# Kernel optimization log

Hardware: AMD Instinct MI355X
Metric: run time of the kernel (lower is better)

The kernel has to match this reference:

```python
import jax, jax.numpy as jnp
import numpy as np

D_MODEL = 1024
N_HEADS = 16
HEAD_DIM = D_MODEL // N_HEADS
EPS = 1e-5


def _rope_tables(T, dim, dtype):
    inv_freq = 1.0 / (10000.0 ** (np.arange(0, dim, 2, dtype=np.float32) / dim))
    t = np.arange(T, dtype=np.float32)
    freqs = np.einsum('i,j->ij', t, inv_freq)            # [T, dim/2]
    emb = np.concatenate([freqs, freqs], axis=-1)        # [T, dim]
    return jnp.asarray(np.cos(emb), dtype), jnp.asarray(np.sin(emb), dtype)


def _rotate(x, cos, sin):
    # x: [B, T, H, hd]; cos/sin: [T, hd] broadcast over B, H
    c = cos[None, :, None, :]
    s = sin[None, :, None, :]
    x1, x2 = jnp.split(x, 2, axis=-1)
    return x * c + jnp.concatenate([-x2, x1], axis=-1) * s


def setup_inputs() -> dict:
    key = jax.random.key(0)
    k1, k2, k3 = jax.random.split(key, 3)
    B, T = 2, 2048
    x = jax.random.normal(k1, (B, T, D_MODEL), jnp.float32)
    norm_w = jnp.ones((D_MODEL,), jnp.float32)
    w_qkv = jax.random.normal(k2, (D_MODEL, 3 * D_MODEL), jnp.float32) * (D_MODEL ** -0.5)
    w_out = jax.random.normal(k3, (D_MODEL, D_MODEL), jnp.float32) * (D_MODEL ** -0.5)
    return {"x": x, "norm_w": norm_w, "w_qkv": w_qkv, "w_out": w_out}


def reference(x, norm_w, w_qkv, w_out):
    B, T, D = x.shape
    residual = x
    # RMSNorm
    h = x * jax.lax.rsqrt(jnp.mean(x * x, axis=-1, keepdims=True) + EPS) * norm_w
    # QKV projection
    qkv = (h @ w_qkv).reshape(B, T, 3, N_HEADS, HEAD_DIM)
    q, k, v = qkv[:, :, 0], qkv[:, :, 1], qkv[:, :, 2]   # [B, T, H, hd]
    # RoPE
    cos, sin = _rope_tables(T, HEAD_DIM, x.dtype)
    q = _rotate(q, cos, sin)
    k = _rotate(k, cos, sin)
    # Non-causal scaled dot-product attention
    scale = HEAD_DIM ** -0.5
    scores = jnp.einsum('bqhd,bkhd->bhqk', q, k) * scale
    attn = jax.nn.softmax(scores, axis=-1)
    out = jnp.einsum('bhqk,bkhd->bqhd', attn, v).reshape(B, T, D)
    return residual + out @ w_out
```

## Files before the change

### kernel.cpp

```cpp
#include <hip/hip_runtime.h>
#include <hip/hip_bf16.h>

typedef float f32x4 __attribute__((ext_vector_type(4)));
typedef __bf16 bf16x8 __attribute__((ext_vector_type(8)));
typedef __bf16 bf16x4 __attribute__((ext_vector_type(4)));

#define D_MODEL 1024
#define T_SEQ   2048
#define NH      16
#define HD      64

__device__ __forceinline__ void gload16(const void* g, void* l) {
    __builtin_amdgcn_global_load_lds(
        (const __attribute__((address_space(1))) unsigned int*)g,
        (__attribute__((address_space(3))) unsigned int*)l, 16, 0, 0);
}

__global__ __launch_bounds__(256) void k_rope_table(float2* __restrict__ tab) {
    int idx = blockIdx.x * 256 + threadIdx.x;
    int t = idx >> 5, i = idx & 31;
    float inv = powf(10000.f, -(float)i * (1.f / 32.f));
    float ang = (float)t * inv;
    tab[idx] = make_float2(cosf(ang), sinf(ang));
}

__global__ __launch_bounds__(256) void k_rmsnorm(const float* __restrict__ x,
                                                 const float* __restrict__ w,
                                                 __bf16* __restrict__ h) {
    int row = blockIdx.x;
    int tid = threadIdx.x;
    const float4 v = ((const float4*)(x + (size_t)row * D_MODEL))[tid];
    float ss = v.x * v.x + v.y * v.y + v.z * v.z + v.w * v.w;
#pragma unroll
    for (int off = 32; off > 0; off >>= 1) ss += __shfl_down(ss, off, 64);
    __shared__ float red[4];
    if ((tid & 63) == 0) red[tid >> 6] = ss;
    __syncthreads();
    float total = red[0] + red[1] + red[2] + red[3];
    float rms = rsqrtf(total * (1.f / 1024.f) + 1e-5f);
    const float4 wv = ((const float4*)w)[tid];
    bf16x4 o;
    o[0] = (__bf16)(v.x * rms * wv.x);
    o[1] = (__bf16)(v.y * rms * wv.y);
    o[2] = (__bf16)(v.z * rms * wv.z);
    o[3] = (__bf16)(v.w * rms * wv.w);
    ((bf16x4*)(h + (size_t)row * D_MODEL))[tid] = o;
}

__global__ __launch_bounds__(256) void k_transpose_cast(const float* __restrict__ src,
                                                        __bf16* __restrict__ dst,
                                                        int R, int C) {
    __shared__ float tile[32][33];
    int tx = threadIdx.x & 31, ty = threadIdx.x >> 5;
    int c0 = blockIdx.x * 32, r0 = blockIdx.y * 32;
#pragma unroll
    for (int dy = 0; dy < 32; dy += 8)
        tile[ty + dy][tx] = src[(size_t)(r0 + ty + dy) * C + c0 + tx];
    __syncthreads();
#pragma unroll
    for (int dy = 0; dy < 32; dy += 8)
        dst[(size_t)(c0 + ty + dy) * R + r0 + tx] = (__bf16)tile[tx][ty + dy];
}

template <int EPI>
__global__ __launch_bounds__(256) void k_gemm(const __bf16* __restrict__ A,
                                              const __bf16* __restrict__ Bt, int K,
                                              const float2* __restrict__ tab,
                                              __bf16* __restrict__ Qr,
                                              __bf16* __restrict__ Kr,
                                              __bf16* __restrict__ Vt,
                                              const float* __restrict__ resid,
                                              float* __restrict__ outf) {
    __shared__ __bf16 ldsA[128 * 64];
    __shared__ __bf16 ldsB[128 * 64];
    const int tid  = threadIdx.x;
    const int lane = tid & 63;
    const int wave = tid >> 6;
    const int tile_m = blockIdx.y * 128;
    const int tile_n = blockIdx.x * 128;
    const int wm = (wave >> 1) * 64;
    const int wn = (wave & 1) * 64;
    f32x4 acc[4][4] = {};

    const int srow8 = lane >> 3;
    const int sslot = lane & 7;

    for (int k0 = 0; k0 < K; k0 += 64) {
#pragma unroll
        for (int i = 0; i < 4; i++) {
            int rbase = i * 32 + wave * 8;
            int row = rbase + srow8;
            int scol = (sslot ^ (row & 7)) * 8;
            gload16(A  + (size_t)(tile_m + row) * K + k0 + scol,
                    (char*)ldsA + rbase * 128);
            gload16(Bt + (size_t)(tile_n + row) * K + k0 + scol,
                    (char*)ldsB + rbase * 128);
        }
        __syncthreads();
#pragma unroll
        for (int kc = 0; kc < 2; kc++) {
            bf16x8 af[4], bfr[4];
            int s = kc * 4 + (lane >> 4);
#pragma unroll
            for (int mi = 0; mi < 4; mi++) {
                int row = wm + mi * 16 + (lane & 15);
                af[mi] = *(const bf16x8*)((char*)ldsA + row * 128 + ((s ^ (row & 7)) << 4));
            }
#pragma unroll
            for (int nf = 0; nf < 4; nf++) {
                int row = wn + nf * 16 + (lane & 15);
                bfr[nf] = *(const bf16x8*)((char*)ldsB + row * 128 + ((s ^ (row & 7)) << 4));
            }
#pragma unroll
            for (int mi = 0; mi < 4; mi++)
#pragma unroll
                for (int nf = 0; nf < 4; nf++)
                    acc[mi][nf] = __builtin_amdgcn_mfma_f32_16x16x32_bf16(
                        af[mi], bfr[nf], acc[mi][nf], 0, 0, 0);
        }
        __syncthreads();
    }

    if (EPI == 0) {
        const int nb  = tile_n + wn;
        const int sec = nb >> 10;
        const int hh  = (nb & 1023) >> 6;
        if (sec < 2) {
            __bf16* dstbase = (sec == 0) ? Qr : Kr;
            const float sc = (sec == 0) ? 0.180336880111f : 1.0f;
#pragma unroll
            for (int mi = 0; mi < 4; mi++) {
#pragma unroll
                for (int r = 0; r < 4; r++) {
                    int m = tile_m + wm + mi * 16 + (lane >> 4) * 4 + r;
                    int bb = m >> 11, t = m & 2047;
                    float2 cs0 = tab[t * 32 + (lane & 15)];
                    float2 cs1 = tab[t * 32 + 16 + (lane & 15)];
                    float x0 = acc[mi][0][r], x1 = acc[mi][1][r];
                    float x2 = acc[mi][2][r], x3 = acc[mi][3][r];
                    __bf16* dst = dstbase + ((size_t)(bb * NH + hh) * T_SEQ + t) * HD + (lane & 15);
                    dst[0]  = (__bf16)((x0 * cs0.x - x2 * cs0.y) * sc);
                    dst[16] = (__bf16)((x1 * cs1.x - x3 * cs1.y) * sc);
                    dst[32] = (__bf16)((x2 * cs0.x + x0 * cs0.y) * sc);
                    dst[48] = (__bf16)((x3 * cs1.x + x1 * cs1.y) * sc);
                }
            }
        } else {
#pragma unroll
            for (int mi = 0; mi < 4; mi++) {
                int m0 = tile_m + wm + mi * 16 + (lane >> 4) * 4;
                int bb = m0 >> 11, t0 = m0 & 2047;
#pragma unroll
                for (int nf = 0; nf < 4; nf++) {
                    int d = nf * 16 + (lane & 15);
                    bf16x4 pv;
                    pv[0] = (__bf16)acc[mi][nf][0];
                    pv[1] = (__bf16)acc[mi][nf][1];
                    pv[2] = (__bf16)acc[mi][nf][2];
                    pv[3] = (__bf16)acc[mi][nf][3];
                    *(bf16x4*)(Vt + ((size_t)(bb * NH + hh) * HD + d) * T_SEQ + t0) = pv;
                }
            }
        }
    } else {
#pragma unroll
        for (int mi = 0; mi < 4; mi++)
#pragma unroll
            for (int r = 0; r < 4; r++) {
                int m = tile_m + wm + mi * 16 + (lane >> 4) * 4 + r;
#pragma unroll
                for (int nf = 0; nf < 4; nf++) {
                    int n = tile_n + wn + nf * 16 + (lane & 15);
                    size_t idx = (size_t)m * D_MODEL + n;
                    outf[idx] = resid[idx] + acc[mi][nf][r];
                }
            }
    }
}

__global__ __launch_bounds__(256, 4) void k_attn(const __bf16* __restrict__ Qr,
                                                 const __bf16* __restrict__ Kr,
                                                 const __bf16* __restrict__ Vt,
                                                 __bf16* __restrict__ aout) {
    __shared__ __bf16 ldsK[2][64 * 64];
    __shared__ __bf16 ldsV[2][64 * 64];
    __shared__ __bf16 plds_all[4][16 * 64];
    const int lane = threadIdx.x & 63;
    const int wave = threadIdx.x >> 6;
    const int g  = lane >> 4;
    const int lr = lane & 15;

    const int lin = blockIdx.x;
    const int xcd = lin & 7;
    const int idx = lin >> 3;
    const int bh  = xcd * 4 + (idx >> 5);
    const int qb  = idx & 31;
    const int q0  = qb * 64 + wave * 16;

    const __bf16* Q  = Qr + (size_t)bh * T_SEQ * HD;
    const __bf16* Kp = Kr + (size_t)bh * T_SEQ * HD;
    const __bf16* Vp = Vt + (size_t)bh * HD * T_SEQ;
    char* plds = (char*)plds_all[wave];

    bf16x8 qf[2];
#pragma unroll
    for (int kc = 0; kc < 2; kc++)
        qf[kc] = *(const bf16x8*)(Q + (size_t)(q0 + lr) * HD + kc * 32 + g * 8);

    const int srow8 = lane >> 3;
    const int sslot = lane & 7;
    auto stage = [&](int buf, int kk) {
#pragma unroll
        for (int j = 0; j < 2; j++) {
            int c = wave * 2 + j;
            int row = c * 8 + srow8;
            int scol = (sslot ^ (row & 7)) * 8;
            gload16(Kp + (size_t)(kk + row) * HD + scol,
                    (char*)&ldsK[buf][0] + c * 1024);
            gload16(Vp + (size_t)row * T_SEQ + kk + scol,
                    (char*)&ldsV[buf][0] + c * 1024);
        }
    };

    f32x4 o[4] = {};
    float mrun = -1e30f;
    float lrun = 0.f;

    stage(0, 0);
    __syncthreads();
    int buf = 0;

    for (int tile = 0; tile < 32; tile++) {
        if (tile < 31) stage(buf ^ 1, (tile + 1) * 64);

        const char* Kb = (const char*)&ldsK[buf][0];
        const char* Vb = (const char*)&ldsV[buf][0];

        f32x4 s[4] = {};
#pragma unroll
        for (int kc = 0; kc < 2; kc++) {
            bf16x8 kf[4];
#pragma unroll
            for (int ki = 0; ki < 4; ki++) {
                int row = ki * 16 + lr;
                kf[ki] = *(const bf16x8*)(Kb + row * 128 +
                                          ((kc * 64 + g * 16) ^ ((row & 7) << 4)));
            }
#pragma unroll
            for (int ki = 0; ki < 4; ki++)
                s[ki] = __builtin_amdgcn_mfma_f32_16x16x32_bf16(
                    kf[ki], qf[kc], s[ki], 0, 0, 0);
        }

        float t0 = fmaxf(fmaxf(s[0][0], s[0][1]), fmaxf(s[0][2], s[0][3]));
        float t1 = fmaxf(fmaxf(s[1][0], s[1][1]), fmaxf(s[1][2], s[1][3]));
        float t2 = fmaxf(fmaxf(s[2][0], s[2][1]), fmaxf(s[2][2], s[2][3]));
        float t3 = fmaxf(fmaxf(s[3][0], s[3][1]), fmaxf(s[3][2], s[3][3]));
        float tv = fmaxf(fmaxf(t0, t1), fmaxf(t2, t3));
        tv = fmaxf(tv, __shfl_xor(tv, 16, 64));
        tv = fmaxf(tv, __shfl_xor(tv, 32, 64));
        float mnew = fmaxf(mrun, tv);
        float fac = __builtin_amdgcn_exp2f(mrun - mnew);
        mrun = mnew;
        float ts = 0.f;
#pragma unroll
        for (int ki = 0; ki < 4; ki++) {
            float p0 = __builtin_amdgcn_exp2f(s[ki][0] - mnew);
            float p1 = __builtin_amdgcn_exp2f(s[ki][1] - mnew);
            float p2 = __builtin_amdgcn_exp2f(s[ki][2] - mnew);
            float p3 = __builtin_amdgcn_exp2f(s[ki][3] - mnew);
            ts += (p0 + p1) + (p2 + p3);
            bf16x4 pk;
            pk[0] = (__bf16)p0; pk[1] = (__bf16)p1;
            pk[2] = (__bf16)p2; pk[3] = (__bf16)p3;
            *(bf16x4*)(plds + lr * 128 + ((ki * 32 + g * 8) ^ ((lr & 7) << 4))) = pk;
        }
        ts += __shfl_xor(ts, 16, 64);
        ts += __shfl_xor(ts, 32, 64);
        lrun = lrun * fac + ts;
        float facT[4];
#pragma unroll
        for (int r = 0; r < 4; r++)
            facT[r] = __shfl(fac, g * 4 + r, 64);
#pragma unroll
        for (int nf = 0; nf < 4; nf++)
#pragma unroll
            for (int r = 0; r < 4; r++)
                o[nf][r] *= facT[r];

#pragma unroll
        for (int kc = 0; kc < 2; kc++) {
            bf16x8 pf = *(const bf16x8*)(plds + lr * 128 +
                                         ((kc * 64 + g * 16) ^ ((lr & 7) << 4)));
            bf16x8 vf[4];
#pragma unroll
            for (int nf = 0; nf < 4; nf++) {
                int row = nf * 16 + lr;
                vf[nf] = *(const bf16x8*)(Vb + row * 128 +
                                          ((kc * 64 + g * 16) ^ ((row & 7) << 4)));
            }
#pragma unroll
            for (int nf = 0; nf < 4; nf++)
                o[nf] = __builtin_amdgcn_mfma_f32_16x16x32_bf16(
                    pf, vf[nf], o[nf], 0, 0, 0);
        }
        __syncthreads();
        buf ^= 1;
    }

    const int bb = bh >> 4, hh = bh & 15;
    float invT[4];
#pragma unroll
    for (int r = 0; r < 4; r++)
        invT[r] = 1.f / __shfl(lrun, g * 4 + r, 64);
#pragma unroll
    for (int r = 0; r < 4; r++) {
        int t = q0 + g * 4 + r;
#pragma unroll
        for (int nf = 0; nf < 4; nf++) {
            int d = nf * 16 + lr;
            aout[((size_t)(bb * T_SEQ + t)) * D_MODEL + hh * HD + d] =
                (__bf16)(o[nf][r] * invT[r]);
        }
    }
}

extern "C" void kernel_launch(void* const* d_in, const int* in_sizes, int n_in,
                              void* d_out, int out_size, void* d_ws, size_t ws_size,
                              hipStream_t stream) {
    const float* x      = (const float*)d_in[0];
    const float* norm_w = (const float*)d_in[1];
    const float* w_qkv  = (const float*)d_in[2];
    const float* w_out  = (const float*)d_in[3];
    float* out = (float*)d_out;
    char* ws = (char*)d_ws;

    __bf16* hbuf  = (__bf16*)(ws);
    __bf16* wqkvT = (__bf16*)(ws + ((size_t)8  << 20));
    __bf16* woutT = (__bf16*)(ws + ((size_t)14 << 20));
    float2* tab   = (float2*)(ws + ((size_t)16 << 20));
    __bf16* Qr    = (__bf16*)(ws + ((size_t)17 << 20));
    __bf16* Kr    = (__bf16*)(ws + ((size_t)25 << 20));
    __bf16* Vt    = (__bf16*)(ws + ((size_t)33 << 20));

    k_rope_table<<<dim3(256), dim3(256), 0, stream>>>(tab);
    k_rmsnorm<<<dim3(4096), dim3(256), 0, stream>>>(x, norm_w, hbuf);
    k_transpose_cast<<<dim3(96, 32), dim3(256), 0, stream>>>(w_qkv, wqkvT, 1024, 3072);
    k_transpose_cast<<<dim3(32, 32), dim3(256), 0, stream>>>(w_out, woutT, 1024, 1024);
    k_gemm<0><<<dim3(24, 32), dim3(256), 0, stream>>>(hbuf, wqkvT, 1024, tab,
                                                      Qr, Kr, Vt, nullptr, nullptr);
    k_attn<<<dim3(1024), dim3(256), 0, stream>>>(Qr, Kr, Vt, hbuf);
    k_gemm<1><<<dim3(8, 32), dim3(256), 0, stream>>>(hbuf, woutT, 1024, nullptr,
                                                     nullptr, nullptr, nullptr, x, out);
}
```

Baseline: 222.4 us.

## Restructure attention inner loop with lazy rescale, precomputed offsets and priorities

Reworks the flash-attention tile loop. LDS swizzle offsets and global staging pointers are computed once instead of per tile, and V fragment loads are issued early so they overlap the softmax. The online-softmax rescale is skipped unless the running max grows by more than a threshold, and s_setprio is raised around the MFMA sections. The RoPE table's powf is replaced with exp2. The lazy rescale lets exponentials go up to 2^8 before renormalising, which adds some risk of precision loss in the bf16 P values.

```diff
diff --git a/kernel.cpp b/kernel.cpp
--- a/kernel.cpp
+++ b/kernel.cpp
@@ -19,7 +19,7 @@
 __global__ __launch_bounds__(256) void k_rope_table(float2* __restrict__ tab) {
     int idx = blockIdx.x * 256 + threadIdx.x;
     int t = idx >> 5, i = idx & 31;
-    float inv = powf(10000.f, -(float)i * (1.f / 32.f));
+    float inv = __builtin_amdgcn_exp2f(-(float)i * 0.41524101186f);
     float ang = (float)t * inv;
     tab[idx] = make_float2(cosf(ang), sinf(ang));
 }
@@ -201,56 +201,77 @@
     const __bf16* Kp = Kr + (size_t)bh * T_SEQ * HD;
     const __bf16* Vp = Vt + (size_t)bh * HD * T_SEQ;
     char* plds = (char*)plds_all[wave];
+    char* Kbase = (char*)&ldsK[0][0];
+    char* Vbase = (char*)&ldsV[0][0];
+
+    int kofs[2][4], vofs[2][4], pwr[4], prd[2];
+#pragma unroll
+    for (int kc = 0; kc < 2; kc++)
+#pragma unroll
+        for (int i = 0; i < 4; i++) {
+            int row = i * 16 + lr;
+            int sw = (kc * 64 + g * 16) ^ ((row & 7) << 4);
+            kofs[kc][i] = row * 128 + sw;
+            vofs[kc][i] = row * 128 + sw;
+        }
+#pragma unroll
+    for (int ki = 0; ki < 4; ki++)
+        pwr[ki] = lr * 128 + ((ki * 32 + g * 8) ^ ((lr & 7) << 4));
+#pragma unroll
+    for (int kc = 0; kc < 2; kc++)
+        prd[kc] = lr * 128 + ((kc * 64 + g * 16) ^ ((lr & 7) << 4));
+
+    const int srow8 = lane >> 3;
+    const int sslot = lane & 7;
+    const int scol = (sslot ^ srow8) * 8;
+    const int c0 = wave * 2, c1 = wave * 2 + 1;
+    const int r0 = c0 * 8 + srow8, r1 = c1 * 8 + srow8;
+    const __bf16* kg0 = Kp + (size_t)r0 * HD + scol;
+    const __bf16* kg1 = Kp + (size_t)r1 * HD + scol;
+    const __bf16* vg0 = Vp + (size_t)r0 * T_SEQ + scol;
+    const __bf16* vg1 = Vp + (size_t)r1 * T_SEQ + scol;
+    char* Kl0 = Kbase + c0 * 1024;
+    char* Kl1 = Kbase + c1 * 1024;
+    char* Vl0 = Vbase + c0 * 1024;
+    char* Vl1 = Vbase + c1 * 1024;
 
     bf16x8 qf[2];
 #pragma unroll
     for (int kc = 0; kc < 2; kc++)
         qf[kc] = *(const bf16x8*)(Q + (size_t)(q0 + lr) * HD + kc * 32 + g * 8);
-
-    const int srow8 = lane >> 3;
-    const int sslot = lane & 7;
-    auto stage = [&](int buf, int kk) {
-#pragma unroll
-        for (int j = 0; j < 2; j++) {
-            int c = wave * 2 + j;
-            int row = c * 8 + srow8;
-            int scol = (sslot ^ (row & 7)) * 8;
-            gload16(Kp + (size_t)(kk + row) * HD + scol,
-                    (char*)&ldsK[buf][0] + c * 1024);
-            gload16(Vp + (size_t)row * T_SEQ + kk + scol,
-                    (char*)&ldsV[buf][0] + c * 1024);
-        }
-    };
 
     f32x4 o[4] = {};
     float mrun = -1e30f;
     float lrun = 0.f;
 
-    stage(0, 0);
+    gload16(kg0, Kl0); gload16(kg1, Kl1);
+    gload16(vg0, Vl0); gload16(vg1, Vl1);
+    kg0 += 64 * HD; kg1 += 64 * HD; vg0 += 64; vg1 += 64;
     __syncthreads();
-    int buf = 0;
 
     for (int tile = 0; tile < 32; tile++) {
-        if (tile < 31) stage(buf ^ 1, (tile + 1) * 64);
-
-        const char* Kb = (const char*)&ldsK[buf][0];
-        const char* Vb = (const char*)&ldsV[buf][0];
+        const int bufoff = (tile & 1) << 13;
+        if (tile < 31) {
+            const int nb = bufoff ^ 8192;
+            gload16(kg0, Kl0 + nb); gload16(kg1, Kl1 + nb);
+            gload16(vg0, Vl0 + nb); gload16(vg1, Vl1 + nb);
+            kg0 += 64 * HD; kg1 += 64 * HD; vg0 += 64; vg1 += 64;
+        }
 
         f32x4 s[4] = {};
+        __builtin_amdgcn_s_setprio(1);
 #pragma unroll
         for (int kc = 0; kc < 2; kc++) {
             bf16x8 kf[4];
 #pragma unroll
-            for (int ki = 0; ki < 4; ki++) {
-                int row = ki * 16 + lr;
-                kf[ki] = *(const bf16x8*)(Kb + row * 128 +
-                                          ((kc * 64 + g * 16) ^ ((row & 7) << 4)));
-            }
+            for (int ki = 0; ki < 4; ki++)
+                kf[ki] = *(const bf16x8*)(Kbase + bufoff + kofs[kc][ki]);
 #pragma unroll
             for (int ki = 0; ki < 4; ki++)
                 s[ki] = __builtin_amdgcn_mfma_f32_16x16x32_bf16(
                     kf[ki], qf[kc], s[ki], 0, 0, 0);
         }
+        __builtin_amdgcn_s_setprio(0);
 
         float t0 = fmaxf(fmaxf(s[0][0], s[0][1]), fmaxf(s[0][2], s[0][3]));
         float t1 = fmaxf(fmaxf(s[1][0], s[1][1]), fmaxf(s[1][2], s[1][3]));
@@ -259,53 +280,57 @@
         float tv = fmaxf(fmaxf(t0, t1), fmaxf(t2, t3));
         tv = fmaxf(tv, __shfl_xor(tv, 16, 64));
         tv = fmaxf(tv, __shfl_xor(tv, 32, 64));
-        float mnew = fmaxf(mrun, tv);
-        float fac = __builtin_amdgcn_exp2f(mrun - mnew);
-        mrun = mnew;
+        if (!__all(tv - mrun <= 8.f)) {
+            float mnew = fmaxf(mrun, tv);
+            float fac = __builtin_amdgcn_exp2f(mrun - mnew);
+            mrun = mnew;
+            float facT[4];
+#pragma unroll
+            for (int r = 0; r < 4; r++)
+                facT[r] = __shfl(fac, g * 4 + r, 64);
+#pragma unroll
+            for (int nf = 0; nf < 4; nf++)
+#pragma unroll
+                for (int r = 0; r < 4; r++)
+                    o[nf][r] *= facT[r];
+            lrun *= fac;
+        }
         float ts = 0.f;
 #pragma unroll
         for (int ki = 0; ki < 4; ki++) {
-            float p0 = __builtin_amdgcn_exp2f(s[ki][0] - mnew);
-            float p1 = __builtin_amdgcn_exp2f(s[ki][1] - mnew);
-            float p2 = __builtin_amdgcn_exp2f(s[ki][2] - mnew);
-            float p3 = __builtin_amdgcn_exp2f(s[ki][3] - mnew);
+            float p0 = __builtin_amdgcn_exp2f(s[ki][0] - mrun);
+            float p1 = __builtin_amdgcn_exp2f(s[ki][1] - mrun);
+            float p2 = __builtin_amdgcn_exp2f(s[ki][2] - mrun);
+            float p3 = __builtin_amdgcn_exp2f(s[ki][3] - mrun);
             ts += (p0 + p1) + (p2 + p3);
             bf16x4 pk;
             pk[0] = (__bf16)p0; pk[1] = (__bf16)p1;
             pk[2] = (__bf16)p2; pk[3] = (__bf16)p3;
-            *(bf16x4*)(plds + lr * 128 + ((ki * 32 + g * 8) ^ ((lr & 7) << 4))) = pk;
-        }
+            *(bf16x4*)(plds + pwr[ki]) = pk;
+        }
+        bf16x8 vf0[4];
+#pragma unroll
+        for (int nf = 0; nf < 4; nf++)
+            vf0[nf] = *(const bf16x8*)(Vbase + bufoff + vofs[0][nf]);
         ts += __shfl_xor(ts, 16, 64);
         ts += __shfl_xor(ts, 32, 64);
-        lrun = lrun * fac + ts;
-        float facT[4];
-#pragma unroll
-        for (int r = 0; r < 4; r++)
-            facT[r] = __shfl(fac, g * 4 + r, 64);
+        lrun += ts;
+
+        __builtin_amdgcn_s_setprio(1);
+        bf16x8 pf0 = *(const bf16x8*)(plds + prd[0]);
+        bf16x8 vf1[4];
 #pragma unroll
         for (int nf = 0; nf < 4; nf++)
-#pragma unroll
-            for (int r = 0; r < 4; r++)
-                o[nf][r] *= facT[r];
-
-#pragma unroll
-        for (int kc = 0; kc < 2; kc++) {
-            bf16x8 pf = *(const bf16x8*)(plds + lr * 128 +
-                                         ((kc * 64 + g * 16) ^ ((lr & 7) << 4)));
-            bf16x8 vf[4];
-#pragma unroll
-            for (int nf = 0; nf < 4; nf++) {
-                int row = nf * 16 + lr;
-                vf[nf] = *(const bf16x8*)(Vb + row * 128 +
-                                          ((kc * 64 + g * 16) ^ ((row & 7) << 4)));
-            }
-#pragma unroll
-            for (int nf = 0; nf < 4; nf++)
-                o[nf] = __builtin_amdgcn_mfma_f32_16x16x32_bf16(
-                    pf, vf[nf], o[nf], 0, 0, 0);
-        }
+            vf1[nf] = *(const bf16x8*)(Vbase + bufoff + vofs[1][nf]);
+#pragma unroll
+        for (int nf = 0; nf < 4; nf++)
+            o[nf] = __builtin_amdgcn_mfma_f32_16x16x32_bf16(pf0, vf0[nf], o[nf], 0, 0, 0);
+        bf16x8 pf1 = *(const bf16x8*)(plds + prd[1]);
+#pragma unroll
+        for (int nf = 0; nf < 4; nf++)
+            o[nf] = __builtin_amdgcn_mfma_f32_16x16x32_bf16(pf1, vf1[nf], o[nf], 0, 0, 0);
+        __builtin_amdgcn_s_setprio(0);
         __syncthreads();
-        buf ^= 1;
     }
 
     const int bb = bh >> 4, hh = bh & 15;
```

After: 216.2 us. 1.03x faster.
